# Kernel optimization log

Measured on AMD Instinct MI355X. Metric: run time of the kernel, lower is better.

The kernel has to match this reference:

```python
import jax, jax.numpy as jnp
import numpy as np

N = 8192          # codeword length (power of 2)
K = 4096          # info bits (rate 1/2)
BS = 8192         # batch of codewords


def _gen_indices(n):
    """Stage-wise gather indices for the Arikan butterfly.
    Row s: position ind_dest XORs with ind_dest + 2**s; all other positions
    gather the sentinel column n, which holds a constant 0 (XOR identity)."""
    nb_stages = int(np.log2(n))
    ind = np.full((nb_stages, n + 1), n, dtype=np.int32)
    for s in range(nb_stages):
        r = np.arange(n // 2)
        ind_dest = r * 2 - (r % (2 ** s))
        ind[s, ind_dest] = ind_dest + 2 ** s
    return ind


def setup_inputs() -> dict:
    key = jax.random.key(0)
    u = jax.random.randint(key, (BS, K), 0, 2).astype(jnp.float32)  # info bits in {0,1}
    frozen_pos = np.arange(N - K)
    info_pos = jnp.asarray(np.setdiff1d(np.arange(N), frozen_pos), dtype=jnp.int32)
    ind_gather = jnp.asarray(_gen_indices(N))  # [log2(N), N+1] int32
    return {"u": u, "info_pos": info_pos, "ind_gather": ind_gather}


def reference(u, info_pos, ind_gather):
    bs = u.shape[0]
    n = ind_gather.shape[1] - 1
    nb_stages = ind_gather.shape[0]
    # scatter info bits into codeword positions (frozen positions stay 0)
    c = jnp.zeros((bs, n), dtype=u.dtype).at[:, info_pos].set(u)
    # append the zero sentinel column used as XOR identity
    x = jnp.concatenate([c, jnp.zeros((bs, 1), dtype=u.dtype)], axis=1)  # [bs, n+1]
    for s in range(nb_stages):  # fixed log2(n) structurally-distinct stages
        x = (x + x[:, ind_gather[s]]) % 2  # XOR on {0,1} bits
    return x[:, :n]
```

## Files before the change

kernel.cpp:

```cpp
#include <hip/hip_runtime.h>


constexpr int ROWS      = 8192;
constexpr int K_WORDS   = 1024;
constexpr int OUT_WORDS = 2048;

__global__ __launch_bounds__(256)
void polar_encode_kernel(const uint4* __restrict__ u, uint4* __restrict__ out) {
    const int lane = threadIdx.x & 63;
    const int row  = (blockIdx.x << 2) + (threadIdx.x >> 6);

    const uint4* urow = u + (size_t)row * K_WORDS;

    uint4 v[16];
#pragma unroll
    for (int r = 0; r < 16; ++r) v[r] = urow[(r << 6) + lane];

#pragma unroll
    for (int r = 0; r < 16; ++r) { v[r].x ^= v[r].y; v[r].z ^= v[r].w; }
#pragma unroll
    for (int r = 0; r < 16; ++r) { v[r].x ^= v[r].z; v[r].y ^= v[r].w; }

#pragma unroll
    for (int s = 0; s < 6; ++s) {
        const unsigned m = ((lane >> s) & 1) ? 0u : 0xFFFFFFFFu;
#pragma unroll
        for (int r = 0; r < 16; ++r) {
            unsigned px = (unsigned)__shfl_xor((int)v[r].x, 1 << s, 64);
            unsigned py = (unsigned)__shfl_xor((int)v[r].y, 1 << s, 64);
            unsigned pz = (unsigned)__shfl_xor((int)v[r].z, 1 << s, 64);
            unsigned pw = (unsigned)__shfl_xor((int)v[r].w, 1 << s, 64);
            v[r].x ^= px & m;
            v[r].y ^= py & m;
            v[r].z ^= pz & m;
            v[r].w ^= pw & m;
        }
    }

#pragma unroll
    for (int s = 0; s < 4; ++s) {
#pragma unroll
        for (int r = 0; r < 16; ++r) {
            if (!(r & (1 << s))) {
                const int p = r | (1 << s);
                v[r].x ^= v[p].x;
                v[r].y ^= v[p].y;
                v[r].z ^= v[p].z;
                v[r].w ^= v[p].w;
            }
        }
    }

    uint4* orow = out + (size_t)row * OUT_WORDS;
#pragma unroll
    for (int r = 0; r < 16; ++r) {
        const int o = (r << 6) + lane;
        orow[o]           = v[r];
        orow[K_WORDS + o] = v[r];
    }
}

extern "C" void kernel_launch(void* const* d_in, const int* in_sizes, int n_in,
                              void* d_out, int out_size, void* d_ws, size_t ws_size,
                              hipStream_t stream) {
    (void)in_sizes; (void)n_in; (void)d_ws; (void)ws_size; (void)out_size;
    const uint4* u = (const uint4*)d_in[0];
    uint4* out = (uint4*)d_out;

    dim3 grid(ROWS / 4);
    dim3 block(256);
    hipLaunchKernelGGL(polar_encode_kernel, grid, block, 0, stream, u, out);
}
```

Measured before the change: 359.2 us.

## Replace cross-lane shuffle butterfly with LDS transpose and in-register XOR stages

Each row now gets one 64-thread block. Each lane loads 16 contiguous quads and does the low butterfly stages in registers, then transposes through swizzled shared memory so the remaining six stages run as register XORs over 64 words per lane. This removes all the wavefront shuffles of the old version. In exchange it adds an LDS round trip and a barrier, raises register pressure with 64+ live words, uses small blocks, and makes the per-lane global loads strided, which may coalesce less well.

```diff
diff --git a/kernel.cpp b/kernel.cpp
--- a/kernel.cpp
+++ b/kernel.cpp
@@ -1,62 +1,66 @@
 #include <hip/hip_runtime.h>
 
 
-constexpr int ROWS      = 8192;
-constexpr int K_WORDS   = 1024;
-constexpr int OUT_WORDS = 2048;
+constexpr int ROWS          = 8192;
+constexpr int K_QUADS       = 1024;
+constexpr int OUT_WORDS_F32 = 8192;
 
-__global__ __launch_bounds__(256)
-void polar_encode_kernel(const uint4* __restrict__ u, uint4* __restrict__ out) {
-    const int lane = threadIdx.x & 63;
-    const int row  = (blockIdx.x << 2) + (threadIdx.x >> 6);
+__global__ __launch_bounds__(64)
+void polar_encode_kernel(const uint4* __restrict__ u, unsigned* __restrict__ out) {
+    __shared__ uint4 lds[1024];
 
-    const uint4* urow = u + (size_t)row * K_WORDS;
+    const int l   = threadIdx.x;
+    const int row = blockIdx.x;
 
+    const uint4* urow = u + (size_t)row * K_QUADS + (size_t)l * 16;
     uint4 v[16];
 #pragma unroll
-    for (int r = 0; r < 16; ++r) v[r] = urow[(r << 6) + lane];
+    for (int r = 0; r < 16; ++r) v[r] = urow[r];
 
 #pragma unroll
     for (int r = 0; r < 16; ++r) { v[r].x ^= v[r].y; v[r].z ^= v[r].w; }
 #pragma unroll
     for (int r = 0; r < 16; ++r) { v[r].x ^= v[r].z; v[r].y ^= v[r].w; }
-
-#pragma unroll
-    for (int s = 0; s < 6; ++s) {
-        const unsigned m = ((lane >> s) & 1) ? 0u : 0xFFFFFFFFu;
-#pragma unroll
-        for (int r = 0; r < 16; ++r) {
-            unsigned px = (unsigned)__shfl_xor((int)v[r].x, 1 << s, 64);
-            unsigned py = (unsigned)__shfl_xor((int)v[r].y, 1 << s, 64);
-            unsigned pz = (unsigned)__shfl_xor((int)v[r].z, 1 << s, 64);
-            unsigned pw = (unsigned)__shfl_xor((int)v[r].w, 1 << s, 64);
-            v[r].x ^= px & m;
-            v[r].y ^= py & m;
-            v[r].z ^= pz & m;
-            v[r].w ^= pw & m;
-        }
-    }
-
 #pragma unroll
     for (int s = 0; s < 4; ++s) {
 #pragma unroll
         for (int r = 0; r < 16; ++r) {
             if (!(r & (1 << s))) {
                 const int p = r | (1 << s);
-                v[r].x ^= v[p].x;
-                v[r].y ^= v[p].y;
-                v[r].z ^= v[p].z;
-                v[r].w ^= v[p].w;
+                v[r].x ^= v[p].x; v[r].y ^= v[p].y;
+                v[r].z ^= v[p].z; v[r].w ^= v[p].w;
             }
         }
     }
 
-    uint4* orow = out + (size_t)row * OUT_WORDS;
 #pragma unroll
-    for (int r = 0; r < 16; ++r) {
-        const int o = (r << 6) + lane;
-        orow[o]           = v[r];
-        orow[K_WORDS + o] = v[r];
+    for (int r = 0; r < 16; ++r)
+        lds[l * 16 + (r ^ (l & 15))] = v[r];
+
+    __syncthreads();
+
+    const unsigned* ldsw = (const unsigned*)lds;
+    unsigned g[64];
+#pragma unroll
+    for (int j = 0; j < 64; ++j) {
+        const int qa = j * 16 + ((l >> 2) ^ (j & 15));
+        g[j] = ldsw[qa * 4 + (l & 3)];
+    }
+
+#pragma unroll
+    for (int s = 0; s < 6; ++s) {
+#pragma unroll
+        for (int j = 0; j < 64; ++j) {
+            if (!(j & (1 << s))) g[j] ^= g[j | (1 << s)];
+        }
+    }
+
+    unsigned* orow = out + (size_t)row * OUT_WORDS_F32;
+#pragma unroll
+    for (int j = 0; j < 64; ++j) {
+        const int o = j * 64 + l;
+        orow[o]        = g[j];
+        orow[4096 + o] = g[j];
     }
 }
 
@@ -65,9 +69,8 @@
                               hipStream_t stream) {
     (void)in_sizes; (void)n_in; (void)d_ws; (void)ws_size; (void)out_size;
     const uint4* u = (const uint4*)d_in[0];
-    uint4* out = (uint4*)d_out;
+    unsigned* out = (unsigned*)d_out;
 
-    dim3 grid(ROWS / 4);
-    dim3 block(256);
-    hipLaunchKernelGGL(polar_encode_kernel, grid, block, 0, stream, u, out);
+    hipLaunchKernelGGL(polar_encode_kernel, dim3(ROWS), dim3(64), 0, stream,
+                       u, out);
 }
```

Result: no change. 365.5 us (+1.7%).
